# Optimization experiments

Hardware: AMD Instinct MI355X
Metric: run time of the kernel (lower is better)

Reference implementation:

```python
import jax, jax.numpy as jnp
import numpy as np

N, K, D = 256, 16, 1024
EPS = 1e-06


def setup_inputs() -> dict:
    key = jax.random.key(0)
    k1, k2, k3, k4 = jax.random.split(key, 4)
    scale = 0.05  # keep pairwise distances in a non-saturated logit range
    return {
        'image_features': jax.random.normal(k1, (N, K, D), jnp.float32) * scale,
        'caption_features': jax.random.normal(k2, (N, K, D), jnp.float32) * scale,
        'image_logsigma': jax.random.normal(k3, (N, D), jnp.float32),
        'caption_logsigma': jax.random.normal(k4, (N, D), jnp.float32),
        'negative_scale': jnp.full((1,), 5.0, jnp.float32),
        'shift': jnp.full((1,), 5.0, jnp.float32),
    }


def _pairwise_cdist(x, y):
    # dist[i, j, k, l] = || x[i, k] - y[j, l] ||_2, computed via Gram expansion
    # to avoid materializing the (N, N, K, K, D) broadcast-difference tensor.
    x2 = jnp.sum(x * x, axis=-1)  # (N, K)
    y2 = jnp.sum(y * y, axis=-1)  # (N, K)
    xy = jnp.einsum('ikd,jld->ijkl', x, y)  # (N, N, K, K)
    sq = x2[:, None, :, None] + y2[None, :, None, :] - 2.0 * xy
    sq = jnp.maximum(sq, 0.0)
    return jnp.sqrt(sq + EPS)


def _nll_sum(dist, negative_scale, shift):
    # dist: (N, N, K, K) -> logits (N, N, K*K)
    n = dist.shape[0]
    kk = dist.shape[2] * dist.shape[3]
    logits = (-negative_scale[0] * dist + shift[0]).reshape(n, n, kk)
    matched = jnp.where(jnp.eye(n, dtype=bool), 1.0, -1.0)[:, :, None]  # (N, N, 1)
    # logsumexp over the stacked (logit, -logit) pair == logaddexp(l, -l)
    inner = logits * matched - jnp.logaddexp(logits, -logits)
    nll = -jax.scipy.special.logsumexp(inner, axis=-1) + jnp.log(jnp.float32(kk))  # (N, N)
    return jnp.sum(nll)  # pos (diag) + neg (off-diag) sums


def reference(image_features, caption_features, image_logsigma, caption_logsigma,
              negative_scale, shift):
    # uniform_lambda = 0, vib_beta = 0 -> loss = i2t + t2i soft-contrastive NLL
    dist = _pairwise_cdist(image_features, caption_features)  # (N, N, K, K)
    i2t = _nll_sum(dist, negative_scale, shift)
    # t2i: anchors/candidates swapped -> transposed pair grid (same per-pair set)
    t2i = _nll_sum(jnp.transpose(dist, (1, 0, 3, 2)), negative_scale, shift)
    return i2t + t2i
```

## Files before the change

### kernel.cpp

```cpp
#include <hip/hip_runtime.h>
#include <hip/hip_bf16.h>
#include <cstdint>


using f32x4 = __attribute__((ext_vector_type(4))) float;
using s16x8 = __attribute__((ext_vector_type(8))) short;

#define DDIM   1024
#define BM     128
#define BN     128
#define BK     64
#define LOGKK  5.5451774444795625f
#define DEPS   1e-6f

__device__ __forceinline__ void gload16(const void* g, void* l) {
  __builtin_amdgcn_global_load_lds((const __attribute__((address_space(1))) void*)g,
                                   (__attribute__((address_space(3))) void*)l, 16, 0, 0);
}

__device__ __forceinline__ unsigned short bf16_rne(float x) {
  uint32_t u = __builtin_bit_cast(uint32_t, x);
  uint32_t r = (u + 0x7FFFu + ((u >> 16) & 1u)) >> 16;
  return (unsigned short)r;
}

__global__ __launch_bounds__(256) void mcsc_prep(
    const float* __restrict__ img, const float* __restrict__ cap,
    unsigned short* __restrict__ Xhi, unsigned short* __restrict__ Yhi,
    float* __restrict__ x2, float* __restrict__ y2, float* __restrict__ out)
{
  int w = blockIdx.x * 4 + (threadIdx.x >> 6);
  int lane = threadIdx.x & 63;
  int isY = w >> 12;
  int row = w & 4095;
  const float* src = (isY ? cap : img) + (size_t)row * DDIM;
  unsigned short* dst = (isY ? Yhi : Xhi) + (size_t)row * DDIM;

  float s = 0.f;
#pragma unroll
  for (int j = 0; j < 4; ++j) {
    int col = (j * 64 + lane) * 4;
    float4 v = *(const float4*)(src + col);
    const float* vp = (const float*)&v;
    unsigned short h[4];
#pragma unroll
    for (int e = 0; e < 4; ++e) { float x = vp[e]; s += x * x; h[e] = bf16_rne(x); }
    *(ushort4*)(dst + col) = make_ushort4(h[0], h[1], h[2], h[3]);
  }
#pragma unroll
  for (int off = 32; off >= 1; off >>= 1) s += __shfl_xor(s, off);
  if (lane == 0) (isY ? y2 : x2)[row] = s;
  if (w == 0 && lane == 0) out[0] = 0.f;
}

__global__ __launch_bounds__(256, 2) void mcsc_main(
    const unsigned short* __restrict__ Xhi, const unsigned short* __restrict__ Yhi,
    const float* __restrict__ x2, const float* __restrict__ y2,
    const float* __restrict__ nsp, const float* __restrict__ shp,
    float* __restrict__ out)
{
  __shared__ __align__(16) char ldsA[2][BM * BK * 2];
  __shared__ __align__(16) char ldsB[2][BN * BK * 2];
  __shared__ float redBuf[4];

  int bid = blockIdx.x;
  int wg = (bid & 7) * 128 + (bid >> 3);
  int bm = wg >> 5, bn = wg & 31;
  int rowBase = bm * BM, colBase = bn * BN;

  int t = threadIdx.x;
  int wid = t >> 6, lane = t & 63;
  int lr = lane & 15, lk = lane >> 4;
  int wr = wid >> 1, wc = wid & 1;
  int waveRow = wr * 64, waveCol = wc * 64;

  f32x4 acc[4][4] = {};

  auto stage = [&](int ks, int b) {
    int koff = ks * BK;
#pragma unroll
    for (int c = 0; c < 4; ++c) {
      int q = c * 4096 + t * 16;
      int row = q >> 7;
      int colb = (q ^ ((row & 7) << 4)) & 127;
      const char* gA = (const char*)(Xhi + (size_t)(rowBase + row) * DDIM + koff) + colb;
      const char* gB = (const char*)(Yhi + (size_t)(colBase + row) * DDIM + koff) + colb;
      gload16(gA, &ldsA[b][0] + c * 4096 + wid * 1024);
      gload16(gB, &ldsB[b][0] + c * 4096 + wid * 1024);
    }
  };

  stage(0, 0);
  __syncthreads();

  for (int ks = 0; ks < 16; ++ks) {
    int cur = ks & 1;
    if (ks < 15) stage(ks + 1, cur ^ 1);

#pragma unroll
    for (int kk = 0; kk < BK; kk += 32) {
      s16x8 af[4], bf[4];
#pragma unroll
      for (int m = 0; m < 4; ++m) {
        int rl = waveRow + m * 16 + lr;
        int addr = rl * 128 + ((((kk + lk * 8) * 2)) ^ ((rl & 7) << 4));
        af[m] = *(const s16x8*)(&ldsA[cur][0] + addr);
      }
#pragma unroll
      for (int n = 0; n < 4; ++n) {
        int rl = waveCol + n * 16 + lr;
        int addr = rl * 128 + ((((kk + lk * 8) * 2)) ^ ((rl & 7) << 4));
        bf[n] = *(const s16x8*)(&ldsB[cur][0] + addr);
      }
#pragma unroll
      for (int m = 0; m < 4; ++m)
#pragma unroll
        for (int n = 0; n < 4; ++n)
          acc[m][n] = __builtin_amdgcn_mfma_f32_16x16x32_bf16(af[m], bf[n], acc[m][n], 0, 0, 0);
    }
    __syncthreads();
  }

  float ns = nsp[0], sh = shp[0];
  float waveAcc = 0.f;
#pragma unroll
  for (int m = 0; m < 4; ++m) {
    int gr0 = rowBase + waveRow + m * 16;
    f32x4 x2v = *(const f32x4*)(x2 + gr0 + lk * 4);
#pragma unroll
    for (int n = 0; n < 4; ++n) {
      int gc0 = colBase + waveCol + n * 16;
      bool diag = ((gr0 >> 4) == (gc0 >> 4));
      float y2c = y2[gc0 + lr];
      float ts = 0.f;
#pragma unroll
      for (int r = 0; r < 4; ++r) {
        float sq = x2v[r] + y2c - 2.f * acc[m][n][r];
        sq = fmaxf(sq, 0.f);
        float dd = __fsqrt_rn(sq + DEPS);
        float l = sh - ns * dd;
        float a = diag ? (2.f * l) : (-2.f * l);
        ts += 1.f / (1.f + __expf(-a));
      }
#pragma unroll
      for (int off = 32; off >= 1; off >>= 1) ts += __shfl_xor(ts, off);
      waveAcc += (LOGKK - __logf(ts));
    }
  }
  if (lane == 0) redBuf[wid] = waveAcc;
  __syncthreads();
  if (t == 0) {
    float bs = redBuf[0] + redBuf[1] + redBuf[2] + redBuf[3];
    atomicAdd(out, 2.f * bs);
  }
}

extern "C" void kernel_launch(void* const* d_in, const int* in_sizes, int n_in,
                              void* d_out, int out_size, void* d_ws, size_t ws_size,
                              hipStream_t stream) {
  const float* img = (const float*)d_in[0];
  const float* cap = (const float*)d_in[1];
  const float* nsp = (const float*)d_in[4];
  const float* shp = (const float*)d_in[5];
  float* out = (float*)d_out;

  char* ws = (char*)d_ws;
  unsigned short* Xhi = (unsigned short*)(ws + (size_t)0);
  unsigned short* Yhi = (unsigned short*)(ws + (size_t)8 * 1024 * 1024);
  float* x2 = (float*)(ws + (size_t)16 * 1024 * 1024);
  float* y2 = (float*)(ws + (size_t)16 * 1024 * 1024 + 16384);

  mcsc_prep<<<dim3(2048), dim3(256), 0, stream>>>(img, cap, Xhi, Yhi, x2, y2, out);
  mcsc_main<<<dim3(1024), dim3(256), 0, stream>>>(Xhi, Yhi, x2, y2, nsp, shp, out);
}
```

Baseline: 138.8 us.

## Enlarge Gram GEMM tiles to 256x256 with 512-thread blocks

Doubles the block tile of the bf16 MFMA Gram computation to 256x256, with 8 waves each computing a 128x64 sub-tile in a single 128KB LDS buffer. The grid shrinks to 256 blocks, one per CU. Staging pointers and swizzle offsets are now computed once outside the k-loop. The aim is to halve global and L2 operand traffic per FLOP and to cut address arithmetic. In exchange the accumulator state doubles, which raises the risk of register spills or AGPR pressure under launch_bounds(512,2), and occupancy drops to one block per CU.

```diff
diff --git a/kernel.cpp b/kernel.cpp
--- a/kernel.cpp
+++ b/kernel.cpp
@@ -7,8 +7,8 @@
 using s16x8 = __attribute__((ext_vector_type(8))) short;
 
 #define DDIM   1024
-#define BM     128
-#define BN     128
+#define BM     256
+#define BN     256
 #define BK     64
 #define LOGKK  5.5451774444795625f
 #define DEPS   1e-6f
@@ -53,40 +53,45 @@
   if (w == 0 && lane == 0) out[0] = 0.f;
 }
 
-__global__ __launch_bounds__(256, 2) void mcsc_main(
+__global__ __launch_bounds__(512, 2) void mcsc_main(
     const unsigned short* __restrict__ Xhi, const unsigned short* __restrict__ Yhi,
     const float* __restrict__ x2, const float* __restrict__ y2,
     const float* __restrict__ nsp, const float* __restrict__ shp,
     float* __restrict__ out)
 {
-  __shared__ __align__(16) char ldsA[2][BM * BK * 2];
-  __shared__ __align__(16) char ldsB[2][BN * BK * 2];
-  __shared__ float redBuf[4];
+  __shared__ __align__(16) char lds[131072];
+  __shared__ float redBuf[8];
 
   int bid = blockIdx.x;
-  int wg = (bid & 7) * 128 + (bid >> 3);
-  int bm = wg >> 5, bn = wg & 31;
+  int wg = (bid & 7) * 32 + (bid >> 3);
+  int bm = wg >> 4, bn = wg & 15;
   int rowBase = bm * BM, colBase = bn * BN;
 
   int t = threadIdx.x;
   int wid = t >> 6, lane = t & 63;
   int lr = lane & 15, lk = lane >> 4;
-  int wr = wid >> 1, wc = wid & 1;
-  int waveRow = wr * 64, waveCol = wc * 64;
+  int wr = wid >> 2, wc = wid & 3;
+  int waveRow = wr * 128, waveCol = wc * 64;
 
-  f32x4 acc[4][4] = {};
+  f32x4 acc[8][4] = {};
+
+  int srow = wid * 8 + (lane >> 3);
+  int scol = (((lane & 7) ^ (lane >> 3)) * 16);
+  const char* aPtr[4];
+  const char* bPtr[4];
+#pragma unroll
+  for (int c = 0; c < 4; ++c) {
+    aPtr[c] = (const char*)(Xhi + (size_t)(rowBase + c * 64 + srow) * DDIM) + scol;
+    bPtr[c] = (const char*)(Yhi + (size_t)(colBase + c * 64 + srow) * DDIM) + scol;
+  }
+  int ldsDst = wid * 1024;
 
   auto stage = [&](int ks, int b) {
-    int koff = ks * BK;
+    int ko = ks * 128;
 #pragma unroll
     for (int c = 0; c < 4; ++c) {
-      int q = c * 4096 + t * 16;
-      int row = q >> 7;
-      int colb = (q ^ ((row & 7) << 4)) & 127;
-      const char* gA = (const char*)(Xhi + (size_t)(rowBase + row) * DDIM + koff) + colb;
-      const char* gB = (const char*)(Yhi + (size_t)(colBase + row) * DDIM + koff) + colb;
-      gload16(gA, &ldsA[b][0] + c * 4096 + wid * 1024);
-      gload16(gB, &ldsB[b][0] + c * 4096 + wid * 1024);
+      gload16(aPtr[c] + ko, lds + b * 32768 + c * 8192 + ldsDst);
+      gload16(bPtr[c] + ko, lds + 65536 + b * 32768 + c * 8192 + ldsDst);
     }
   };
 
@@ -97,23 +102,25 @@
     int cur = ks & 1;
     if (ks < 15) stage(ks + 1, cur ^ 1);
 
+    const char* ldsA = lds + cur * 32768;
+    const char* ldsB = lds + 65536 + cur * 32768;
+    int swz = (lr & 7) << 4;
 #pragma unroll
     for (int kk = 0; kk < BK; kk += 32) {
-      s16x8 af[4], bf[4];
+      int kb = (kk + lk * 8) * 2;
+      s16x8 af[8], bf[4];
 #pragma unroll
-      for (int m = 0; m < 4; ++m) {
+      for (int m = 0; m < 8; ++m) {
         int rl = waveRow + m * 16 + lr;
-        int addr = rl * 128 + ((((kk + lk * 8) * 2)) ^ ((rl & 7) << 4));
-        af[m] = *(const s16x8*)(&ldsA[cur][0] + addr);
+        af[m] = *(const s16x8*)(ldsA + rl * 128 + (kb ^ swz));
       }
 #pragma unroll
       for (int n = 0; n < 4; ++n) {
         int rl = waveCol + n * 16 + lr;
-        int addr = rl * 128 + ((((kk + lk * 8) * 2)) ^ ((rl & 7) << 4));
-        bf[n] = *(const s16x8*)(&ldsB[cur][0] + addr);
+        bf[n] = *(const s16x8*)(ldsB + rl * 128 + (kb ^ swz));
       }
 #pragma unroll
-      for (int m = 0; m < 4; ++m)
+      for (int m = 0; m < 8; ++m)
 #pragma unroll
         for (int n = 0; n < 4; ++n)
           acc[m][n] = __builtin_amdgcn_mfma_f32_16x16x32_bf16(af[m], bf[n], acc[m][n], 0, 0, 0);
@@ -124,7 +131,7 @@
   float ns = nsp[0], sh = shp[0];
   float waveAcc = 0.f;
 #pragma unroll
-  for (int m = 0; m < 4; ++m) {
+  for (int m = 0; m < 8; ++m) {
     int gr0 = rowBase + waveRow + m * 16;
     f32x4 x2v = *(const f32x4*)(x2 + gr0 + lk * 4);
 #pragma unroll
@@ -150,7 +157,8 @@
   if (lane == 0) redBuf[wid] = waveAcc;
   __syncthreads();
   if (t == 0) {
-    float bs = redBuf[0] + redBuf[1] + redBuf[2] + redBuf[3];
+    float bs = redBuf[0] + redBuf[1] + redBuf[2] + redBuf[3]
+             + redBuf[4] + redBuf[5] + redBuf[6] + redBuf[7];
     atomicAdd(out, 2.f * bs);
   }
 }
@@ -171,5 +179,5 @@
   float* y2 = (float*)(ws + (size_t)16 * 1024 * 1024 + 16384);
 
   mcsc_prep<<<dim3(2048), dim3(256), 0, stream>>>(img, cap, Xhi, Yhi, x2, y2, out);
-  mcsc_main<<<dim3(1024), dim3(256), 0, stream>>>(Xhi, Yhi, x2, y2, nsp, shp, out);
+  mcsc_main<<<dim3(256), dim3(512), 0, stream>>>(Xhi, Yhi, x2, y2, nsp, shp, out);
 }
```

Result: faster. 133.2 us (-4.0%).
